# Performance work log

Measured on AMD Instinct MI355X. Metric: run time of the kernel, lower is better.

The kernel has to match this reference:

```python
import jax, jax.numpy as jnp
import numpy as np

N_BLOCKS, N_LAYERS = 3, 10
RW, SW = 256, 128          # residual_width, skip_width
COND_DIM = 16
OUT_CH = 256
K = 3                      # kernel_size (odd)
B, L = 1, 4096             # L divisible by max dilation 512
NL = N_BLOCKS * N_LAYERS
DILATIONS = [2 ** l for _ in range(N_BLOCKS) for l in range(N_LAYERS)] + [1]


def dilate(x, new, old):
    # WaveNet dilate trick: (n, c, l) -> (n*new/old, c, l*old/new) by
    # permute->reshape->permute (matches torch permute(1,2,0).view(c,l2,n2).permute(2,0,1)).
    n, c, l = x.shape
    if new == old:
        return x
    n2 = n * new // old
    l2 = l * old // new
    return jnp.transpose(jnp.transpose(x, (1, 2, 0)).reshape(c, l2, n2), (2, 0, 1))


def conv1d(x, w, b=None, pad=0):
    y = jax.lax.conv_general_dilated(x, w, (1,), [(pad, pad)],
                                     dimension_numbers=('NCH', 'OIH', 'NCH'))
    if b is not None:
        y = y + b[None, :, None]
    return y


def setup_inputs() -> dict:
    key = jax.random.key(0)
    ks = jax.random.split(key, 14)
    s = 0.05
    return {
        'x': jax.random.normal(ks[0], (B, 1, L), jnp.float32),
        'conditionals': jax.random.normal(ks[1], (B, COND_DIM, L), jnp.float32),
        'init_w': jax.random.normal(ks[2], (RW, 1, K), jnp.float32) * s,
        'init_b': jnp.zeros((RW,), jnp.float32),
        'init_skip_w': jax.random.normal(ks[3], (SW, RW, 1), jnp.float32) * s,
        'init_skip_b': jnp.zeros((SW,), jnp.float32),
        'filter_w': jax.random.normal(ks[4], (NL, RW, RW, K), jnp.float32) * s,
        'gate_w': jax.random.normal(ks[5], (NL, RW, RW, K), jnp.float32) * s,
        'skip_w': jax.random.normal(ks[6], (NL, SW, RW, 1), jnp.float32) * s,
        'feat_w': jax.random.normal(ks[7], (NL, RW, RW, 1), jnp.float32) * s,
        'fcond_w': jax.random.normal(ks[8], (NL, RW, COND_DIM, 1), jnp.float32) * s,
        'gcond_w': jax.random.normal(ks[9], (NL, RW, COND_DIM, 1), jnp.float32) * s,
        'final_skip_w': jax.random.normal(ks[10], (SW, SW, 1), jnp.float32) * s,
        'final_skip_b': jnp.zeros((SW,), jnp.float32),
        'final_w': jax.random.normal(ks[11], (OUT_CH, SW, 1), jnp.float32) * s,
        'final_b': jnp.zeros((OUT_CH,), jnp.float32),
    }


def reference(x, conditionals, init_w, init_b, init_skip_w, init_skip_b,
              filter_w, gate_w, skip_w, feat_w, fcond_w, gcond_w,
              final_skip_w, final_skip_b, final_w, final_b):
    pad = (K - 1) // 2
    feat = conv1d(x, init_w, init_b, pad=pad)          # (B, RW, L)
    skip = conv1d(feat, init_skip_w, init_skip_b)       # (B, SW, L)
    for i in range(NL):
        d = DILATIONS[i]
        dilated = dilate(feat, d, DILATIONS[i - 1])     # (B*d, RW, L/d)
        f = conv1d(dilated, filter_w[i], pad=pad)
        g = conv1d(dilated, gate_w[i], pad=pad)
        # 1x1 conditioning convs (no bias) on (B, COND_DIM, L), then dilate to match
        cf = jnp.einsum('oi,bil->bol', fcond_w[i, :, :, 0], conditionals)
        cg = jnp.einsum('oi,bil->bol', gcond_w[i, :, :, 0], conditionals)
        f = f + dilate(cf, d, 1)
        g = g + dilate(cg, d, 1)
        residual = jax.nn.sigmoid(f) * jnp.tanh(g)
        feat = dilated + conv1d(residual, feat_w[i])    # residual connection
        skip = skip + dilate(conv1d(residual, skip_w[i]), 1, d)  # undilate skip
    skip = conv1d(jax.nn.relu(skip), final_skip_w, final_skip_b)
    out = conv1d(jax.nn.relu(skip), final_w, final_b)   # (B, OUT_CH, L)
    return out
```

## Files before the change

kernel.cpp:

```cpp
#include <hip/hip_runtime.h>
#include <cstddef>
#include <cstdint>

#define L_LEN 4096
#define RWID 256
#define SWID 128
#define NLAY 30

typedef __attribute__((ext_vector_type(8))) short bf16x8;
typedef __attribute__((ext_vector_type(4))) float f32x4;

__device__ __forceinline__ ushort f2bf(float x) {
  union { float f; uint32_t u; } v; v.f = x;
  uint32_t r = v.u + 0x7fffu + ((v.u >> 16) & 1u);
  return (ushort)(r >> 16);
}

__device__ __forceinline__ void gload16(const void* g, void* l) {
  __builtin_amdgcn_global_load_lds(
      (const __attribute__((address_space(1))) void*)g,
      (__attribute__((address_space(3))) void*)l, 16, 0, 0);
}

__device__ __forceinline__ f32x4 mfma16(bf16x8 a, bf16x8 b, f32x4 c) {
  return __builtin_amdgcn_mfma_f32_16x16x32_bf16(a, b, c, 0, 0, 0);
}

template<int N> __device__ __forceinline__ void waitvm() {
  asm volatile("s_waitcnt vmcnt(%0)" :: "i"(N) : "memory");
}
__device__ __forceinline__ void blockbar() {
  __builtin_amdgcn_sched_barrier(0);
  asm volatile("s_barrier" ::: "memory");
  __builtin_amdgcn_sched_barrier(0);
}

__global__ __launch_bounds__(256) void prep_wres(
    const float* __restrict__ filter_w, const float* __restrict__ gate_w,
    const float* __restrict__ fcond_w, const float* __restrict__ gcond_w,
    ushort* __restrict__ wres)
{
  const int idx = blockIdx.x * 256 + threadIdx.x;
  const int k = idx % 800;
  int rest = idx / 800;
  const int co = rest & 255; rest >>= 8;
  const int fg = rest & 1;
  const int i = rest >> 1;
  float v;
  if (k < 768) {
    const int tap = k >> 8, cin = k & 255;
    const float* s = fg ? gate_w : filter_w;
    v = s[(((size_t)i * 256 + co) * 256 + cin) * 3 + tap];
  } else if (k < 784) {
    const float* s = fg ? gcond_w : fcond_w;
    v = s[((size_t)i * 256 + co) * 16 + (k - 768)];
  } else v = 0.f;
  wres[idx] = f2bf(v);
}

__global__ __launch_bounds__(256) void prep_wu(
    const float* __restrict__ feat_w, const float* __restrict__ skip_w,
    ushort* __restrict__ wu)
{
  const int idx = blockIdx.x * 256 + threadIdx.x;
  const int rc = idx & 255;
  const int rest = idx >> 8;
  const int m = rest % 384;
  const int i = rest / 384;
  float v = (m < 256) ? feat_w[((size_t)i * 256 + m) * 256 + rc]
                      : skip_w[((size_t)i * 128 + (m - 256)) * 256 + rc];
  wu[idx] = f2bf(v);
}

__global__ __launch_bounds__(256) void prep_misc(
    const float* __restrict__ cond, const float* __restrict__ isw,
    const float* __restrict__ fsw, const float* __restrict__ fw,
    ushort* __restrict__ condT, ushort* __restrict__ wisk,
    ushort* __restrict__ wfsk, ushort* __restrict__ wfin,
    ushort* __restrict__ zerobuf)
{
  const int idx = blockIdx.x * 256 + threadIdx.x;
  if (idx < 131072) {
    const int t = idx >> 5, cd = idx & 31;
    condT[idx] = (cd < 16) ? f2bf(cond[(size_t)cd * L_LEN + t]) : (ushort)0;
  } else if (idx < 131072 + 32768) {
    const int j = idx - 131072; wisk[j] = f2bf(isw[j]);
  } else if (idx < 131072 + 32768 + 16384) {
    const int j = idx - (131072 + 32768); wfsk[j] = f2bf(fsw[j]);
  } else if (idx < 131072 + 32768 + 16384 + 32768) {
    const int j = idx - (131072 + 32768 + 16384); wfin[j] = f2bf(fw[j]);
  } else if (idx < 131072 + 32768 + 16384 + 32768 + 512) {
    zerobuf[idx - (131072 + 32768 + 16384 + 32768)] = 0;
  }
}

__global__ __launch_bounds__(256) void init_feat(
    const float* __restrict__ x, const float* __restrict__ w,
    const float* __restrict__ b, float* __restrict__ featT_f32,
    ushort* __restrict__ featT_bf16)
{
  const int t = blockIdx.x, c = threadIdx.x;
  const float xm = (t > 0) ? x[t - 1] : 0.f;
  const float x0 = x[t];
  const float xp = (t < L_LEN - 1) ? x[t + 1] : 0.f;
  const float v = b[c] + w[c * 3] * xm + w[c * 3 + 1] * x0 + w[c * 3 + 2] * xp;
  featT_f32[(size_t)t * 256 + c] = v;
  featT_bf16[(size_t)t * 256 + c] = f2bf(v);
}

__global__ __launch_bounds__(256) void residual_mfma(
    const ushort* __restrict__ featT,
    const ushort* __restrict__ condT,
    const ushort* __restrict__ wres,
    const ushort* __restrict__ zerobuf,
    ushort* __restrict__ resT,
    int d)
{
  __shared__ ushort lds[3][4096];
  const int t0  = blockIdx.x * 64;
  const int co0 = blockIdx.y * 32;
  const int tid = threadIdx.x;
  const int lane = tid & 63;
  const int w    = tid >> 6;

  const int srow = lane >> 2;
  const int soct = (lane & 3) ^ ((srow >> 1) & 3);

  const int fgA  = w >> 1;
  const int arow = ((w & 1) << 4) + srow;
  const ushort* asrc0 = wres + ((size_t)fgA * 256 + (co0 + arow)) * 800 + soct * 8;
  const int aLds = fgA * 1024 + (w & 1) * 512;
  const int bLds = 2048 + w * 512;

  const int rl   = lane & 15;
  const int octr = (lane >> 4) ^ ((rl >> 1) & 3);
  const int aoff = rl * 32 + octr * 8;
  const int boff = 2048 + (w * 16 + rl) * 32 + octr * 8;

  f32x4 accf[2] = {}; f32x4 accg[2] = {};

  auto stage = [&](int kc, int buf) {
    const int k0 = kc * 32;
    gload16(asrc0 + k0, &lds[buf][aLds]);
    const int rB = w * 16 + srow;
    const ushort* bsrc;
    if (kc < 24) {
      const int tap = kc >> 3, cin0 = (kc & 7) * 32;
      const int tt = t0 + rB + (tap - 1) * d;
      bsrc = (tt >= 0 && tt < L_LEN)
               ? featT + (size_t)tt * 256 + cin0 + soct * 8
               : zerobuf;
    } else {
      bsrc = condT + (size_t)(t0 + rB) * 32 + soct * 8;
    }
    gload16(bsrc, &lds[buf][bLds]);
  };

  stage(0, 0);
  stage(1, 1);
  for (int kc = 0; kc < 25; ++kc) {
    if (kc + 2 < 25) { stage(kc + 2, (kc + 2) % 3); waitvm<4>(); }
    else if (kc + 1 < 25) waitvm<2>();
    else waitvm<0>();
    blockbar();
    const ushort* base = lds[kc % 3];
    bf16x8 af0 = *(const bf16x8*)(base + aoff);
    bf16x8 af1 = *(const bf16x8*)(base + aoff + 512);
    bf16x8 ag0 = *(const bf16x8*)(base + aoff + 1024);
    bf16x8 ag1 = *(const bf16x8*)(base + aoff + 1536);
    bf16x8 b0  = *(const bf16x8*)(base + boff);
    accf[0] = mfma16(af0, b0, accf[0]);
    accf[1] = mfma16(af1, b0, accf[1]);
    accg[0] = mfma16(ag0, b0, accg[0]);
    accg[1] = mfma16(ag1, b0, accg[1]);
    blockbar();
  }

  const int cobase = co0 + (lane >> 4) * 4;
  const int t = t0 + w * 16 + rl;
#pragma unroll
  for (int m = 0; m < 2; ++m) {
    const f32x4 f = accf[m], g = accg[m];
    ushort4 ov;
    float o[4];
#pragma unroll
    for (int r = 0; r < 4; ++r) {
      const float ff = f[r], gg = g[r];
      const float sig = 1.f / (1.f + __expf(-ff));
      const float ag2 = fabsf(gg);
      float th = 1.f - 2.f / (__expf(2.f * ag2) + 1.f);
      th = (gg < 0.f) ? -th : th;
      o[r] = sig * th;
    }
    ov.x = f2bf(o[0]); ov.y = f2bf(o[1]); ov.z = f2bf(o[2]); ov.w = f2bf(o[3]);
    *(ushort4*)&resT[(size_t)t * 256 + cobase + m * 16] = ov;
  }
}

__global__ __launch_bounds__(256) void update_mfma(
    const ushort* __restrict__ resT,
    const ushort* __restrict__ wu,
    float* __restrict__ featT_f32, ushort* __restrict__ featT_bf16,
    float* __restrict__ skipT_f32)
{
  __shared__ ushort lds[3][3072];
  const int t0 = blockIdx.x * 64;
  const int m0 = blockIdx.y * 32;
  const int tid = threadIdx.x;
  const int lane = tid & 63;
  const int w    = tid >> 6;

  const int srow = lane >> 2;
  const int soct = (lane & 3) ^ ((srow >> 1) & 3);

  const ushort* asrc0 = wu + (size_t)(m0 + (w & 1) * 16 + srow) * 256 + soct * 8;
  const int aLds = (w & 1) * 512;
  const int bLds = 1024 + w * 512;

  const int rl   = lane & 15;
  const int octr = (lane >> 4) ^ ((rl >> 1) & 3);
  const int aoff = rl * 32 + octr * 8;
  const int boff = 1024 + (w * 16 + rl) * 32 + octr * 8;

  f32x4 acc[2] = {};
  const bool twoLoads = (w < 2);

  auto stage = [&](int kc, int buf) {
    const int k0 = kc * 32;
    if (w < 2) gload16(asrc0 + k0, &lds[buf][aLds]);
    const int rB = w * 16 + srow;
    gload16(resT + (size_t)(t0 + rB) * 256 + k0 + soct * 8, &lds[buf][bLds]);
  };

  stage(0, 0);
  stage(1, 1);
  for (int kc = 0; kc < 8; ++kc) {
    if (kc + 2 < 8) {
      stage(kc + 2, (kc + 2) % 3);
      if (twoLoads) waitvm<4>(); else waitvm<2>();
    } else if (kc + 1 < 8) {
      if (twoLoads) waitvm<2>(); else waitvm<1>();
    } else waitvm<0>();
    blockbar();
    const ushort* base = lds[kc % 3];
    bf16x8 a0 = *(const bf16x8*)(base + aoff);
    bf16x8 a1 = *(const bf16x8*)(base + aoff + 512);
    bf16x8 b0 = *(const bf16x8*)(base + boff);
    acc[0] = mfma16(a0, b0, acc[0]);
    acc[1] = mfma16(a1, b0, acc[1]);
    blockbar();
  }

  const int mbase = m0 + (lane >> 4) * 4;
  const int t = t0 + w * 16 + rl;
#pragma unroll
  for (int m = 0; m < 2; ++m) {
    const int mm = mbase + m * 16;
    const f32x4 a = acc[m];
    if (m0 < 256) {
      float4* p = (float4*)&featT_f32[(size_t)t * 256 + mm];
      float4 v = *p;
      v.x += a[0]; v.y += a[1]; v.z += a[2]; v.w += a[3];
      *p = v;
      ushort4 ov; ov.x = f2bf(v.x); ov.y = f2bf(v.y); ov.z = f2bf(v.z); ov.w = f2bf(v.w);
      *(ushort4*)&featT_bf16[(size_t)t * 256 + mm] = ov;
    } else {
      float4* p = (float4*)&skipT_f32[(size_t)t * 128 + (mm - 256)];
      float4 v = *p;
      v.x += a[0]; v.y += a[1]; v.z += a[2]; v.w += a[3];
      *p = v;
    }
  }
}

template<int MODE, int KLEN>
__global__ __launch_bounds__(256) void gemm_mfma(
    const ushort* __restrict__ A,
    const ushort* __restrict__ B,
    const float* __restrict__ bias,
    void* __restrict__ outp)
{
  __shared__ ushort lds[3][3072];
  const int t0 = blockIdx.x * 64;
  const int m0 = blockIdx.y * 32;
  const int tid = threadIdx.x;
  const int lane = tid & 63;
  const int w    = tid >> 6;

  const int srow = lane >> 2;
  const int soct = (lane & 3) ^ ((srow >> 1) & 3);

  const ushort* asrc0 = A + (size_t)(m0 + (w & 1) * 16 + srow) * KLEN + soct * 8;
  const int aLds = (w & 1) * 512;
  const int bLds = 1024 + w * 512;

  const int rl   = lane & 15;
  const int octr = (lane >> 4) ^ ((rl >> 1) & 3);
  const int aoff = rl * 32 + octr * 8;
  const int boff = 1024 + (w * 16 + rl) * 32 + octr * 8;

  f32x4 acc[2] = {};
  constexpr int NC = KLEN / 32;
  const bool twoLoads = (w < 2);

  auto stage = [&](int kc, int buf) {
    const int k0 = kc * 32;
    if (w < 2) gload16(asrc0 + k0, &lds[buf][aLds]);
    const int rB = w * 16 + srow;
    gload16(B + (size_t)(t0 + rB) * KLEN + k0 + soct * 8, &lds[buf][bLds]);
  };

  stage(0, 0);
  stage(1, 1);
  for (int kc = 0; kc < NC; ++kc) {
    if (kc + 2 < NC) {
      stage(kc + 2, (kc + 2) % 3);
      if (twoLoads) waitvm<4>(); else waitvm<2>();
    } else if (kc + 1 < NC) {
      if (twoLoads) waitvm<2>(); else waitvm<1>();
    } else waitvm<0>();
    blockbar();
    const ushort* base = lds[kc % 3];
    bf16x8 a0 = *(const bf16x8*)(base + aoff);
    bf16x8 a1 = *(const bf16x8*)(base + aoff + 512);
    bf16x8 b0 = *(const bf16x8*)(base + boff);
    acc[0] = mfma16(a0, b0, acc[0]);
    acc[1] = mfma16(a1, b0, acc[1]);
    blockbar();
  }

  const int mbase = m0 + (lane >> 4) * 4;
  const int t = t0 + w * 16 + rl;
#pragma unroll
  for (int m = 0; m < 2; ++m) {
    const int mm = mbase + m * 16;
    const float4 bb = *(const float4*)&bias[mm];
    const f32x4 a = acc[m];
    float o[4] = {a[0] + bb.x, a[1] + bb.y, a[2] + bb.z, a[3] + bb.w};
    if (MODE == 0) {
      *(float4*)&((float*)outp)[(size_t)t * 128 + mm] = make_float4(o[0], o[1], o[2], o[3]);
    } else if (MODE == 1) {
      ushort4 ov;
      ov.x = f2bf(fmaxf(o[0], 0.f)); ov.y = f2bf(fmaxf(o[1], 0.f));
      ov.z = f2bf(fmaxf(o[2], 0.f)); ov.w = f2bf(fmaxf(o[3], 0.f));
      *(ushort4*)&((ushort*)outp)[(size_t)t * 128 + mm] = ov;
    } else {
      float* op = (float*)outp;
#pragma unroll
      for (int r = 0; r < 4; ++r) op[(size_t)(mm + r) * L_LEN + t] = o[r];
    }
  }
}

__global__ __launch_bounds__(256) void relu_cvt(
    const float* __restrict__ in, ushort* __restrict__ outv, int n4)
{
  const int i = blockIdx.x * 256 + threadIdx.x;
  if (i >= n4) return;
  const float4 v = ((const float4*)in)[i];
  ushort4 o;
  o.x = f2bf(fmaxf(v.x, 0.f)); o.y = f2bf(fmaxf(v.y, 0.f));
  o.z = f2bf(fmaxf(v.z, 0.f)); o.w = f2bf(fmaxf(v.w, 0.f));
  ((ushort4*)outv)[i] = o;
}

extern "C" void kernel_launch(void* const* d_in, const int* in_sizes, int n_in,
                              void* d_out, int out_size, void* d_ws, size_t ws_size,
                              hipStream_t stream) {
  const float* x            = (const float*)d_in[0];
  const float* cond         = (const float*)d_in[1];
  const float* init_w       = (const float*)d_in[2];
  const float* init_b       = (const float*)d_in[3];
  const float* init_skip_w  = (const float*)d_in[4];
  const float* init_skip_b  = (const float*)d_in[5];
  const float* filter_w     = (const float*)d_in[6];
  const float* gate_w       = (const float*)d_in[7];
  const float* skip_w       = (const float*)d_in[8];
  const float* feat_w       = (const float*)d_in[9];
  const float* fcond_w      = (const float*)d_in[10];
  const float* gcond_w      = (const float*)d_in[11];
  const float* final_skip_w = (const float*)d_in[12];
  const float* final_skip_b = (const float*)d_in[13];
  const float* final_w      = (const float*)d_in[14];
  const float* final_b      = (const float*)d_in[15];
  float* out = (float*)d_out;
  (void)in_sizes; (void)n_in; (void)out_size; (void)ws_size;

  char* ws = (char*)d_ws;
  size_t off = 0;
  auto alloc = [&](size_t bytes) { void* p = ws + off; off = (off + bytes + 255) & ~(size_t)255; return p; };
  float*  featT_f32  = (float*) alloc((size_t)L_LEN * 256 * 4);
  ushort* featT_bf16 = (ushort*)alloc((size_t)L_LEN * 256 * 2);
  ushort* resT       = (ushort*)alloc((size_t)L_LEN * 256 * 2);
  float*  skipT_f32  = (float*) alloc((size_t)L_LEN * 128 * 4);
  ushort* skipR      = (ushort*)alloc((size_t)L_LEN * 128 * 2);
  ushort* skip2R     = (ushort*)alloc((size_t)L_LEN * 128 * 2);
  ushort* condT      = (ushort*)alloc((size_t)L_LEN * 32 * 2);
  ushort* wres       = (ushort*)alloc((size_t)NLAY * 2 * 256 * 800 * 2);
  ushort* wu         = (ushort*)alloc((size_t)NLAY * 384 * 256 * 2);
  ushort* wisk       = (ushort*)alloc((size_t)128 * 256 * 2);
  ushort* wfsk       = (ushort*)alloc((size_t)128 * 128 * 2);
  ushort* wfin       = (ushort*)alloc((size_t)256 * 128 * 2);
  ushort* zerobuf    = (ushort*)alloc(1024);

  const dim3 B256(256);
  prep_wres<<<48000, B256, 0, stream>>>(filter_w, gate_w, fcond_w, gcond_w, wres);
  prep_wu<<<11520, B256, 0, stream>>>(feat_w, skip_w, wu);
  prep_misc<<<833, B256, 0, stream>>>(cond, init_skip_w, final_skip_w, final_w,
                                      condT, wisk, wfsk, wfin, zerobuf);
  init_feat<<<L_LEN, B256, 0, stream>>>(x, init_w, init_b, featT_f32, featT_bf16);
  gemm_mfma<0, 256><<<dim3(64, 4), B256, 0, stream>>>(wisk, featT_bf16, init_skip_b, skipT_f32);

  for (int i = 0; i < NLAY; ++i) {
    const int d = 1 << (i % 10);
    residual_mfma<<<dim3(64, 8), B256, 0, stream>>>(
        featT_bf16, condT, wres + (size_t)i * 2 * 256 * 800, zerobuf, resT, d);
    update_mfma<<<dim3(64, 12), B256, 0, stream>>>(
        resT, wu + (size_t)i * 384 * 256, featT_f32, featT_bf16, skipT_f32);
  }

  relu_cvt<<<512, B256, 0, stream>>>(skipT_f32, skipR, (L_LEN * 128) / 4);
  gemm_mfma<1, 128><<<dim3(64, 4), B256, 0, stream>>>(wfsk, skipR, final_skip_b, skip2R);
  gemm_mfma<2, 128><<<dim3(64, 8), B256, 0, stream>>>(wfin, skip2R, final_b, out);
}
```

Measured before the change: 635.0 us.

## Double K-chunk depth to 64 in residual and update GEMMs, fuse relu conversion

The residual and update MFMA kernels now stage 64-wide K chunks instead of 32. This halves the number of pipeline iterations and barriers per tile. The weight and condition layouts are re-padded (KPAD 832, condT width 64) to fit, and the LDS swizzle changes to an 8-way XOR pattern. The standalone relu_cvt pass is folded into the last update kernel's skip epilogue. The cost is doubled LDS per block, which may lower occupancy, plus some extra zero-padded MACs on the conditioning chunk.

```diff
diff --git a/kernel.cpp b/kernel.cpp
--- a/kernel.cpp
+++ b/kernel.cpp
@@ -6,6 +6,7 @@
 #define RWID 256
 #define SWID 128
 #define NLAY 30
+#define KPAD 832
 
 typedef __attribute__((ext_vector_type(8))) short bf16x8;
 typedef __attribute__((ext_vector_type(4))) float f32x4;
@@ -41,21 +42,28 @@
     ushort* __restrict__ wres)
 {
   const int idx = blockIdx.x * 256 + threadIdx.x;
-  const int k = idx % 800;
-  int rest = idx / 800;
-  const int co = rest & 255; rest >>= 8;
-  const int fg = rest & 1;
-  const int i = rest >> 1;
-  float v;
-  if (k < 768) {
-    const int tap = k >> 8, cin = k & 255;
+  const int T1 = NLAY * 2 * 256 * 256;
+  if (idx < T1) {
+    const int cin = idx & 255;
+    const int co  = (idx >> 8) & 255;
+    const int fg  = (idx >> 16) & 1;
+    const int i   = idx >> 17;
     const float* s = fg ? gate_w : filter_w;
-    v = s[(((size_t)i * 256 + co) * 256 + cin) * 3 + tap];
-  } else if (k < 784) {
-    const float* s = fg ? gcond_w : fcond_w;
-    v = s[((size_t)i * 256 + co) * 16 + (k - 768)];
-  } else v = 0.f;
-  wres[idx] = f2bf(v);
+    const size_t rb = (((size_t)i * 256 + co) * 256 + cin) * 3;
+    const size_t wb = ((size_t)(i * 2 + fg) * 256 + co) * KPAD + cin;
+    wres[wb]       = f2bf(s[rb]);
+    wres[wb + 256] = f2bf(s[rb + 1]);
+    wres[wb + 512] = f2bf(s[rb + 2]);
+  } else {
+    const int j = idx - T1;
+    const int kz = j & 63;
+    const int co = (j >> 6) & 255;
+    const int fg = (j >> 14) & 1;
+    const int i  = j >> 15;
+    const float* cw = fg ? gcond_w : fcond_w;
+    const float v = (kz < 16) ? cw[((size_t)i * 256 + co) * 16 + kz] : 0.f;
+    wres[((size_t)(i * 2 + fg) * 256 + co) * KPAD + 768 + kz] = f2bf(v);
+  }
 }
 
 __global__ __launch_bounds__(256) void prep_wu(
@@ -80,17 +88,17 @@
     ushort* __restrict__ zerobuf)
 {
   const int idx = blockIdx.x * 256 + threadIdx.x;
-  if (idx < 131072) {
-    const int t = idx >> 5, cd = idx & 31;
+  if (idx < 262144) {
+    const int t = idx >> 6, cd = idx & 63;
     condT[idx] = (cd < 16) ? f2bf(cond[(size_t)cd * L_LEN + t]) : (ushort)0;
-  } else if (idx < 131072 + 32768) {
-    const int j = idx - 131072; wisk[j] = f2bf(isw[j]);
-  } else if (idx < 131072 + 32768 + 16384) {
-    const int j = idx - (131072 + 32768); wfsk[j] = f2bf(fsw[j]);
-  } else if (idx < 131072 + 32768 + 16384 + 32768) {
-    const int j = idx - (131072 + 32768 + 16384); wfin[j] = f2bf(fw[j]);
-  } else if (idx < 131072 + 32768 + 16384 + 32768 + 512) {
-    zerobuf[idx - (131072 + 32768 + 16384 + 32768)] = 0;
+  } else if (idx < 262144 + 32768) {
+    const int j = idx - 262144; wisk[j] = f2bf(isw[j]);
+  } else if (idx < 262144 + 32768 + 16384) {
+    const int j = idx - (262144 + 32768); wfsk[j] = f2bf(fsw[j]);
+  } else if (idx < 262144 + 32768 + 16384 + 32768) {
+    const int j = idx - (262144 + 32768 + 16384); wfin[j] = f2bf(fw[j]);
+  } else if (idx < 262144 + 32768 + 16384 + 32768 + 512) {
+    zerobuf[idx - (262144 + 32768 + 16384 + 32768)] = 0;
   }
 }
 
@@ -116,67 +124,74 @@
     ushort* __restrict__ resT,
     int d)
 {
-  __shared__ ushort lds[3][4096];
+  __shared__ ushort lds[3][8192];
   const int t0  = blockIdx.x * 64;
   const int co0 = blockIdx.y * 32;
   const int tid = threadIdx.x;
   const int lane = tid & 63;
   const int w    = tid >> 6;
 
-  const int srow = lane >> 2;
-  const int soct = (lane & 3) ^ ((srow >> 1) & 3);
-
-  const int fgA  = w >> 1;
-  const int arow = ((w & 1) << 4) + srow;
-  const ushort* asrc0 = wres + ((size_t)fgA * 256 + (co0 + arow)) * 800 + soct * 8;
-  const int aLds = fgA * 1024 + (w & 1) * 512;
-  const int bLds = 2048 + w * 512;
-
-  const int rl   = lane & 15;
-  const int octr = (lane >> 4) ^ ((rl >> 1) & 3);
-  const int aoff = rl * 32 + octr * 8;
-  const int boff = 2048 + (w * 16 + rl) * 32 + octr * 8;
+  const int srow8 = lane >> 3;
+  const int soct  = (lane & 7) ^ srow8;
+  const int rl = lane & 15;
+  const int hi = lane >> 4;
+  const int sw = rl & 7;
 
   f32x4 accf[2] = {}; f32x4 accg[2] = {};
 
   auto stage = [&](int kc, int buf) {
-    const int k0 = kc * 32;
-    gload16(asrc0 + k0, &lds[buf][aLds]);
-    const int rB = w * 16 + srow;
-    const ushort* bsrc;
-    if (kc < 24) {
-      const int tap = kc >> 3, cin0 = (kc & 7) * 32;
-      const int tt = t0 + rB + (tap - 1) * d;
-      bsrc = (tt >= 0 && tt < L_LEN)
-               ? featT + (size_t)tt * 256 + cin0 + soct * 8
-               : zerobuf;
+    const int k0 = kc * 64;
+    if (w < 2) {
+#pragma unroll
+      for (int j = 0; j < 4; ++j) {
+        const int r = j * 8 + srow8;
+        gload16(wres + ((size_t)w * 256 + co0 + r) * KPAD + k0 + soct * 8,
+                &lds[buf][(w * 32 + j * 8) * 64]);
+      }
     } else {
-      bsrc = condT + (size_t)(t0 + rB) * 32 + soct * 8;
-    }
-    gload16(bsrc, &lds[buf][bLds]);
+#pragma unroll
+      for (int j = 0; j < 4; ++j) {
+        const int r = (w - 2) * 32 + j * 8 + srow8;
+        const ushort* src;
+        if (kc < 12) {
+          const int tap = kc >> 2, cin0 = (kc & 3) * 64;
+          const int tt = t0 + r + (tap - 1) * d;
+          src = (tt >= 0 && tt < L_LEN)
+                  ? featT + (size_t)tt * 256 + cin0 + soct * 8
+                  : zerobuf;
+        } else {
+          src = condT + (size_t)(t0 + r) * 64 + soct * 8;
+        }
+        gload16(src, &lds[buf][4096 + ((w - 2) * 32 + j * 8) * 64]);
+      }
+    }
   };
 
   stage(0, 0);
   stage(1, 1);
-  for (int kc = 0; kc < 25; ++kc) {
-    if (kc + 2 < 25) { stage(kc + 2, (kc + 2) % 3); waitvm<4>(); }
-    else if (kc + 1 < 25) waitvm<2>();
+  for (int kc = 0; kc < 13; ++kc) {
+    if (kc + 2 < 13) { stage(kc + 2, (kc + 2) % 3); waitvm<8>(); }
+    else if (kc + 1 < 13) waitvm<4>();
     else waitvm<0>();
     blockbar();
     const ushort* base = lds[kc % 3];
-    bf16x8 af0 = *(const bf16x8*)(base + aoff);
-    bf16x8 af1 = *(const bf16x8*)(base + aoff + 512);
-    bf16x8 ag0 = *(const bf16x8*)(base + aoff + 1024);
-    bf16x8 ag1 = *(const bf16x8*)(base + aoff + 1536);
-    bf16x8 b0  = *(const bf16x8*)(base + boff);
-    accf[0] = mfma16(af0, b0, accf[0]);
-    accf[1] = mfma16(af1, b0, accf[1]);
-    accg[0] = mfma16(ag0, b0, accg[0]);
-    accg[1] = mfma16(ag1, b0, accg[1]);
-    blockbar();
-  }
-
-  const int cobase = co0 + (lane >> 4) * 4;
+#pragma unroll
+    for (int kk = 0; kk < 2; ++kk) {
+      const int oct = (hi + kk * 4) ^ sw;
+      bf16x8 b0  = *(const bf16x8*)(base + 4096 + (w * 16 + rl) * 64 + oct * 8);
+      bf16x8 af0 = *(const bf16x8*)(base + (rl) * 64 + oct * 8);
+      bf16x8 af1 = *(const bf16x8*)(base + (16 + rl) * 64 + oct * 8);
+      bf16x8 ag0 = *(const bf16x8*)(base + (32 + rl) * 64 + oct * 8);
+      bf16x8 ag1 = *(const bf16x8*)(base + (48 + rl) * 64 + oct * 8);
+      accf[0] = mfma16(af0, b0, accf[0]);
+      accf[1] = mfma16(af1, b0, accf[1]);
+      accg[0] = mfma16(ag0, b0, accg[0]);
+      accg[1] = mfma16(ag1, b0, accg[1]);
+    }
+    blockbar();
+  }
+
+  const int cobase = co0 + hi * 4;
   const int t = t0 + w * 16 + rl;
 #pragma unroll
   for (int m = 0; m < 2; ++m) {
@@ -201,57 +216,59 @@
     const ushort* __restrict__ resT,
     const ushort* __restrict__ wu,
     float* __restrict__ featT_f32, ushort* __restrict__ featT_bf16,
-    float* __restrict__ skipT_f32)
-{
-  __shared__ ushort lds[3][3072];
+    float* __restrict__ skipT_f32, ushort* __restrict__ skipR)
+{
+  __shared__ ushort lds[3][6144];
   const int t0 = blockIdx.x * 64;
   const int m0 = blockIdx.y * 32;
   const int tid = threadIdx.x;
   const int lane = tid & 63;
   const int w    = tid >> 6;
 
-  const int srow = lane >> 2;
-  const int soct = (lane & 3) ^ ((srow >> 1) & 3);
-
-  const ushort* asrc0 = wu + (size_t)(m0 + (w & 1) * 16 + srow) * 256 + soct * 8;
-  const int aLds = (w & 1) * 512;
-  const int bLds = 1024 + w * 512;
-
-  const int rl   = lane & 15;
-  const int octr = (lane >> 4) ^ ((rl >> 1) & 3);
-  const int aoff = rl * 32 + octr * 8;
-  const int boff = 1024 + (w * 16 + rl) * 32 + octr * 8;
+  const int srow8 = lane >> 3;
+  const int soct  = (lane & 7) ^ srow8;
+  const int rl = lane & 15;
+  const int hi = lane >> 4;
+  const int sw = rl & 7;
 
   f32x4 acc[2] = {};
-  const bool twoLoads = (w < 2);
 
   auto stage = [&](int kc, int buf) {
-    const int k0 = kc * 32;
-    if (w < 2) gload16(asrc0 + k0, &lds[buf][aLds]);
-    const int rB = w * 16 + srow;
-    gload16(resT + (size_t)(t0 + rB) * 256 + k0 + soct * 8, &lds[buf][bLds]);
+    const int k0 = kc * 64;
+    {
+      const int r = w * 8 + srow8;
+      gload16(wu + (size_t)(m0 + r) * 256 + k0 + soct * 8,
+              &lds[buf][(w * 8) * 64]);
+    }
+#pragma unroll
+    for (int j = 0; j < 2; ++j) {
+      const int r = w * 16 + j * 8 + srow8;
+      gload16(resT + (size_t)(t0 + r) * 256 + k0 + soct * 8,
+              &lds[buf][2048 + (w * 16 + j * 8) * 64]);
+    }
   };
 
   stage(0, 0);
   stage(1, 1);
-  for (int kc = 0; kc < 8; ++kc) {
-    if (kc + 2 < 8) {
-      stage(kc + 2, (kc + 2) % 3);
-      if (twoLoads) waitvm<4>(); else waitvm<2>();
-    } else if (kc + 1 < 8) {
-      if (twoLoads) waitvm<2>(); else waitvm<1>();
-    } else waitvm<0>();
+  for (int kc = 0; kc < 4; ++kc) {
+    if (kc + 2 < 4) { stage(kc + 2, (kc + 2) % 3); waitvm<6>(); }
+    else if (kc + 1 < 4) waitvm<3>();
+    else waitvm<0>();
     blockbar();
     const ushort* base = lds[kc % 3];
-    bf16x8 a0 = *(const bf16x8*)(base + aoff);
-    bf16x8 a1 = *(const bf16x8*)(base + aoff + 512);
-    bf16x8 b0 = *(const bf16x8*)(base + boff);
-    acc[0] = mfma16(a0, b0, acc[0]);
-    acc[1] = mfma16(a1, b0, acc[1]);
-    blockbar();
-  }
-
-  const int mbase = m0 + (lane >> 4) * 4;
+#pragma unroll
+    for (int kk = 0; kk < 2; ++kk) {
+      const int oct = (hi + kk * 4) ^ sw;
+      bf16x8 b0 = *(const bf16x8*)(base + 2048 + (w * 16 + rl) * 64 + oct * 8);
+      bf16x8 a0 = *(const bf16x8*)(base + (rl) * 64 + oct * 8);
+      bf16x8 a1 = *(const bf16x8*)(base + (16 + rl) * 64 + oct * 8);
+      acc[0] = mfma16(a0, b0, acc[0]);
+      acc[1] = mfma16(a1, b0, acc[1]);
+    }
+    blockbar();
+  }
+
+  const int mbase = m0 + hi * 4;
   const int t = t0 + w * 16 + rl;
 #pragma unroll
   for (int m = 0; m < 2; ++m) {
@@ -269,6 +286,12 @@
       float4 v = *p;
       v.x += a[0]; v.y += a[1]; v.z += a[2]; v.w += a[3];
       *p = v;
+      if (skipR) {
+        ushort4 sv;
+        sv.x = f2bf(fmaxf(v.x, 0.f)); sv.y = f2bf(fmaxf(v.y, 0.f));
+        sv.z = f2bf(fmaxf(v.z, 0.f)); sv.w = f2bf(fmaxf(v.w, 0.f));
+        *(ushort4*)&skipR[(size_t)t * 128 + (mm - 256)] = sv;
+      }
     }
   }
 }
@@ -350,18 +373,6 @@
       for (int r = 0; r < 4; ++r) op[(size_t)(mm + r) * L_LEN + t] = o[r];
     }
   }
-}
-
-__global__ __launch_bounds__(256) void relu_cvt(
-    const float* __restrict__ in, ushort* __restrict__ outv, int n4)
-{
-  const int i = blockIdx.x * 256 + threadIdx.x;
-  if (i >= n4) return;
-  const float4 v = ((const float4*)in)[i];
-  ushort4 o;
-  o.x = f2bf(fmaxf(v.x, 0.f)); o.y = f2bf(fmaxf(v.y, 0.f));
-  o.z = f2bf(fmaxf(v.z, 0.f)); o.w = f2bf(fmaxf(v.w, 0.f));
-  ((ushort4*)outv)[i] = o;
 }
 
 extern "C" void kernel_launch(void* const* d_in, const int* in_sizes, int n_in,
@@ -395,8 +406,8 @@
   float*  skipT_f32  = (float*) alloc((size_t)L_LEN * 128 * 4);
   ushort* skipR      = (ushort*)alloc((size_t)L_LEN * 128 * 2);
   ushort* skip2R     = (ushort*)alloc((size_t)L_LEN * 128 * 2);
-  ushort* condT      = (ushort*)alloc((size_t)L_LEN * 32 * 2);
-  ushort* wres       = (ushort*)alloc((size_t)NLAY * 2 * 256 * 800 * 2);
+  ushort* condT      = (ushort*)alloc((size_t)L_LEN * 64 * 2);
+  ushort* wres       = (ushort*)alloc((size_t)NLAY * 2 * 256 * KPAD * 2);
   ushort* wu         = (ushort*)alloc((size_t)NLAY * 384 * 256 * 2);
   ushort* wisk       = (ushort*)alloc((size_t)128 * 256 * 2);
   ushort* wfsk       = (ushort*)alloc((size_t)128 * 128 * 2);
@@ -404,22 +415,22 @@
   ushort* zerobuf    = (ushort*)alloc(1024);
 
   const dim3 B256(256);
-  prep_wres<<<48000, B256, 0, stream>>>(filter_w, gate_w, fcond_w, gcond_w, wres);
+  prep_wres<<<19200, B256, 0, stream>>>(filter_w, gate_w, fcond_w, gcond_w, wres);
   prep_wu<<<11520, B256, 0, stream>>>(feat_w, skip_w, wu);
-  prep_misc<<<833, B256, 0, stream>>>(cond, init_skip_w, final_skip_w, final_w,
-                                      condT, wisk, wfsk, wfin, zerobuf);
+  prep_misc<<<1346, B256, 0, stream>>>(cond, init_skip_w, final_skip_w, final_w,
+                                       condT, wisk, wfsk, wfin, zerobuf);
   init_feat<<<L_LEN, B256, 0, stream>>>(x, init_w, init_b, featT_f32, featT_bf16);
   gemm_mfma<0, 256><<<dim3(64, 4), B256, 0, stream>>>(wisk, featT_bf16, init_skip_b, skipT_f32);
 
   for (int i = 0; i < NLAY; ++i) {
     const int d = 1 << (i % 10);
     residual_mfma<<<dim3(64, 8), B256, 0, stream>>>(
-        featT_bf16, condT, wres + (size_t)i * 2 * 256 * 800, zerobuf, resT, d);
+        featT_bf16, condT, wres + (size_t)i * 2 * 256 * KPAD, zerobuf, resT, d);
     update_mfma<<<dim3(64, 12), B256, 0, stream>>>(
-        resT, wu + (size_t)i * 384 * 256, featT_f32, featT_bf16, skipT_f32);
-  }
-
-  relu_cvt<<<512, B256, 0, stream>>>(skipT_f32, skipR, (L_LEN * 128) / 4);
+        resT, wu + (size_t)i * 384 * 256, featT_f32, featT_bf16, skipT_f32,
+        (i == NLAY - 1) ? skipR : (ushort*)nullptr);
+  }
+
   gemm_mfma<1, 128><<<dim3(64, 4), B256, 0, stream>>>(wfsk, skipR, final_skip_b, skip2R);
   gemm_mfma<2, 128><<<dim3(64, 8), B256, 0, stream>>>(wfin, skip2R, final_b, out);
 }
```

Result: no change. 638.3 us (+0.5%).
